# Kernel tuning notes

Measured on AMD Instinct MI355X. Metric: run time of the kernel, lower is better.

## Reference

```python
import jax, jax.numpy as jnp
import numpy as np

B, T_SRC, T_TGT, C_IN, C_OUT = 8, 4096, 2048, 1024, 1024
LN_EPS = 1e-5


def _prefix_mask(lens, T):
    return (jnp.arange(T)[None, :] < lens[:, None]).astype(jnp.int32)


def setup_inputs() -> dict:
    key = jax.random.key(0)
    ks = jax.random.split(key, 6)
    src = jax.random.normal(ks[0], (B, T_SRC, C_IN), dtype=jnp.float32)
    tgt = jax.random.normal(ks[1], (B, T_TGT, C_IN), dtype=jnp.float32)
    # ragged prefix lengths; first row full so src_sizes.max() == T_SRC (static result width)
    src_lens = jax.random.randint(ks[2], (B,), T_SRC // 2, T_SRC + 1).at[0].set(T_SRC)
    tgt_lens = jax.random.randint(ks[3], (B,), T_TGT // 2, T_TGT + 1).at[0].set(T_TGT)
    src_mask = _prefix_mask(src_lens, T_SRC)
    tgt_mask = _prefix_mask(tgt_lens, T_TGT)
    conv_w = jax.random.normal(ks[4], (C_OUT, C_IN), dtype=jnp.float32) * 0.02
    conv_b = jax.random.normal(ks[5], (C_OUT,), dtype=jnp.float32) * 0.02
    ln_g = jnp.ones((C_OUT,), dtype=jnp.float32)
    ln_b = jnp.zeros((C_OUT,), dtype=jnp.float32)
    return {"src": src, "src_mask": src_mask, "tgt": tgt, "tgt_mask": tgt_mask,
            "conv_w": conv_w, "conv_b": conv_b, "ln_g": ln_g, "ln_b": ln_b}


def reference(src, src_mask, tgt, tgt_mask, conv_w, conv_b, ln_g, ln_b):
    # kernel-size-1 Conv1d == per-token linear: [B,T_tgt,C_in] @ W^T + b
    y = jnp.einsum("btc,oc->bto", tgt, conv_w) + conv_b  # [B, T_tgt, C_out]

    src_sizes = src_mask.sum(-1).astype(jnp.int32)  # [B]
    tgt_sizes = tgt_mask.sum(-1).astype(jnp.int32)  # [B]

    # Batched nearest-neighbor ragged resize: out pos j maps to floor(j*tgt/src)
    j = jnp.arange(src.shape[1], dtype=jnp.int32)  # [T_src]
    safe_src = jnp.maximum(src_sizes, 1)[:, None]
    idx = (j[None, :] * tgt_sizes[:, None]) // safe_src  # [B, T_src]
    idx = jnp.clip(idx, 0, jnp.maximum(tgt_sizes, 1)[:, None] - 1)
    gathered = jnp.take_along_axis(y, idx[:, :, None], axis=1)  # [B, T_src, C_out]
    valid = (j[None, :] < src_sizes[:, None])[:, :, None]
    upsampled = jnp.where(valid, gathered, 0.0)

    # LayerNorm over channel dim (applied to all positions, incl. zero padding, as in torch)
    mu = upsampled.mean(-1, keepdims=True)
    var = jnp.mean(jnp.square(upsampled - mu), axis=-1, keepdims=True)
    out = (upsampled - mu) * jax.lax.rsqrt(var + LN_EPS) * ln_g + ln_b
    return (out, src_mask)
```

## Files before the change

kernel.cpp:

```cpp
#include <hip/hip_runtime.h>

#define NB   8
#define TSRC 4096
#define TTGT 2048
#define CH   1024
#define BK   64

typedef __attribute__((ext_vector_type(4))) float  f32x4;
typedef __attribute__((ext_vector_type(8))) __bf16 bf16x8;
typedef __attribute__((ext_vector_type(4))) __bf16 bf16x4;

__device__ __forceinline__ void async16(const void* g, void* l) {
  __builtin_amdgcn_global_load_lds((const __attribute__((address_space(1))) void*)g,
                                   (__attribute__((address_space(3))) void*)l, 16, 0, 0);
}

__global__ __launch_bounds__(256) void prep_kernel(const float* __restrict__ W,
                                                   const int* __restrict__ src_mask,
                                                   const int* __restrict__ tgt_mask,
                                                   __bf16* __restrict__ Wbf,
                                                   int* __restrict__ sizes,
                                                   float* __restrict__ mask_out) {
  const int bx = blockIdx.x;
  const int t  = threadIdx.x;
  if (bx < CH) {
    const float4 v = ((const float4*)(W + (size_t)bx * CH))[t];
    bf16x4 u = {(__bf16)v.x, (__bf16)v.y, (__bf16)v.z, (__bf16)v.w};
    *(bf16x4*)(Wbf + (size_t)bx * CH + t * 4) = u;
  } else if (bx < CH + 16) {
    const int id = bx - CH;
    const int b  = id & 7;
    const int* m = (id < 8) ? (src_mask + (size_t)b * TSRC) : (tgt_mask + (size_t)b * TTGT);
    const int T  = (id < 8) ? TSRC : TTGT;
    int s = 0;
    for (int i = t; i < T; i += 256) s += m[i];
#pragma unroll
    for (int off = 32; off > 0; off >>= 1) s += __shfl_down(s, off);
    __shared__ int red[4];
    if ((t & 63) == 0) red[t >> 6] = s;
    __syncthreads();
    if (t == 0) sizes[id] = red[0] + red[1] + red[2] + red[3];
  } else {
    const int i = (bx - (CH + 16)) * 256 + t;
    mask_out[i] = (float)src_mask[i];
  }
}

__global__ __launch_bounds__(256) void gemm_kernel(const float* __restrict__ A32,
                                                   const __bf16* __restrict__ Bw,
                                                   const float* __restrict__ bias,
                                                   const int* __restrict__ sizes,
                                                   __bf16* __restrict__ y) {
  const int bid = blockIdx.x;
  const int Mt  = bid & 127;
  const int Nt  = bid >> 7;
  const int n0 = Nt * 128;
  const int m0 = Mt * 128;
  const int b  = m0 >> 11;
  const int t0 = m0 & (TTGT - 1);
  if (t0 >= sizes[8 + b]) return;

  __shared__ __bf16 As[128 * BK];
  __shared__ __bf16 Bs[128 * BK];

  const int tid  = threadIdx.x;
  const int lane = tid & 63;
  const int wave = tid >> 6;
  const int wm   = (wave >> 1) * 64;
  const int wn   = (wave & 1) * 64;
  const int lr   = lane & 15;
  const int quad = lane >> 4;

  const int srow = tid >> 3;
  const int scol = (tid & 7) * 8;
  const float*  gA = A32 + (size_t)(m0 + srow) * CH + scol;
  const __bf16* gB = Bw  + (size_t)(n0 + srow) * CH + scol;
  __bf16* lA = As + tid * 8;
  __bf16* lB = Bs + tid * 8;

  f32x4 acc[4][4];
  const f32x4 z = {0.f, 0.f, 0.f, 0.f};
#pragma unroll
  for (int i = 0; i < 4; ++i)
#pragma unroll
    for (int j = 0; j < 4; ++j) acc[i][j] = z;

  float4 a0[4], a1[4];

#pragma unroll
  for (int q = 0; q < 4; ++q) {
    const float* p = gA + (size_t)q * 32 * CH;
    a0[q] = *(const float4*)p;
    a1[q] = *(const float4*)(p + 4);
  }
#pragma unroll
  for (int q = 0; q < 4; ++q) {
    bf16x8 u = {(__bf16)a0[q].x, (__bf16)a0[q].y, (__bf16)a0[q].z, (__bf16)a0[q].w,
                (__bf16)a1[q].x, (__bf16)a1[q].y, (__bf16)a1[q].z, (__bf16)a1[q].w};
    *(bf16x8*)(lA + q * 2048) = u;
  }
#pragma unroll
  for (int q = 0; q < 4; ++q) async16(gB + (size_t)q * 32 * CH, lB + q * 2048);
  __syncthreads();

  for (int kt = 0; kt < CH / BK; ++kt) {
    const int nkb  = (kt + 1) * BK;
    const bool more = (nkb < CH);
    if (more) {
#pragma unroll
      for (int q = 0; q < 4; ++q) {
        const float* p = gA + (size_t)q * 32 * CH + nkb;
        a0[q] = *(const float4*)p;
        a1[q] = *(const float4*)(p + 4);
      }
    }
#pragma unroll
    for (int ko = 0; ko < 2; ++ko) {
      bf16x8 af[4], bf[4];
#pragma unroll
      for (int i = 0; i < 4; ++i)
        af[i] = *(const bf16x8*)(As + (wm + i * 16 + lr) * BK + ko * 32 + quad * 8);
#pragma unroll
      for (int j = 0; j < 4; ++j)
        bf[j] = *(const bf16x8*)(Bs + (wn + j * 16 + lr) * BK + ko * 32 + quad * 8);
#pragma unroll
      for (int i = 0; i < 4; ++i)
#pragma unroll
        for (int j = 0; j < 4; ++j)
          acc[i][j] = __builtin_amdgcn_mfma_f32_16x16x32_bf16(af[i], bf[j], acc[i][j], 0, 0, 0);
    }
    __syncthreads();
    if (more) {
#pragma unroll
      for (int q = 0; q < 4; ++q) {
        bf16x8 u = {(__bf16)a0[q].x, (__bf16)a0[q].y, (__bf16)a0[q].z, (__bf16)a0[q].w,
                    (__bf16)a1[q].x, (__bf16)a1[q].y, (__bf16)a1[q].z, (__bf16)a1[q].w};
        *(bf16x8*)(lA + q * 2048) = u;
      }
#pragma unroll
      for (int q = 0; q < 4; ++q) async16(gB + (size_t)q * 32 * CH + nkb, lB + q * 2048);
    }
    __syncthreads();
  }

#pragma unroll
  for (int i = 0; i < 4; ++i) {
    const int mrow = m0 + wm + i * 16 + quad * 4;
#pragma unroll
    for (int j = 0; j < 4; ++j) {
      const int ncol = n0 + wn + j * 16 + lr;
      const float bv = bias[ncol];
      __bf16* yp = y + (size_t)mrow * CH + ncol;
#pragma unroll
      for (int r = 0; r < 4; ++r) yp[(size_t)r * CH] = (__bf16)(acc[i][j][r] + bv);
    }
  }
}

__global__ __launch_bounds__(256) void ln_kernel(const __bf16* __restrict__ y,
                                                 const int* __restrict__ sizes,
                                                 const float* __restrict__ g,
                                                 const float* __restrict__ be,
                                                 float* __restrict__ out) {
  const int wid = (blockIdx.x * 256 + threadIdx.x) >> 6;
  const int l   = threadIdx.x & 63;
#pragma unroll
  for (int rr = 0; rr < 4; ++rr) {
    const int row = wid + rr * 8192;
    const int b   = row >> 12;
    const int j   = row & (TSRC - 1);
    const int ss  = sizes[b];
    const int tg  = sizes[8 + b];
    float v[16];
    if (j < ss) {
      const int den = (ss > 0) ? ss : 1;
      int ii = (int)(((long long)j * (long long)tg) / den);
      const int hi = ((tg > 1) ? tg : 1) - 1;
      ii = (ii > hi) ? hi : ((ii < 0) ? 0 : ii);
      const __bf16* yr = y + ((size_t)b * TTGT + ii) * CH;
      const bf16x8 u0 = *(const bf16x8*)(yr + l * 8);
      const bf16x8 u1 = *(const bf16x8*)(yr + 512 + l * 8);
#pragma unroll
      for (int k = 0; k < 8; ++k) { v[k] = (float)u0[k]; v[8 + k] = (float)u1[k]; }
    } else {
#pragma unroll
      for (int k = 0; k < 16; ++k) v[k] = 0.f;
    }
    float s = 0.f, q = 0.f;
#pragma unroll
    for (int k = 0; k < 16; ++k) { s += v[k]; q += v[k] * v[k]; }
#pragma unroll
    for (int off = 32; off > 0; off >>= 1) {
      s += __shfl_xor(s, off);
      q += __shfl_xor(q, off);
    }
    const float mu = s * (1.0f / CH);
    float var = q * (1.0f / CH) - mu * mu;
    var = fmaxf(var, 0.0f);
    const float rs = rsqrtf(var + 1e-5f);
    float* orow = out + (size_t)row * CH;
#pragma unroll
    for (int h = 0; h < 2; ++h) {
      const int base = h * 512 + l * 8;
      const float4 g0 = *(const float4*)(g + base);
      const float4 g1 = *(const float4*)(g + base + 4);
      const float4 b0 = *(const float4*)(be + base);
      const float4 b1 = *(const float4*)(be + base + 4);
      float4 o0, o1;
      o0.x = (v[h * 8 + 0] - mu) * rs * g0.x + b0.x;
      o0.y = (v[h * 8 + 1] - mu) * rs * g0.y + b0.y;
      o0.z = (v[h * 8 + 2] - mu) * rs * g0.z + b0.z;
      o0.w = (v[h * 8 + 3] - mu) * rs * g0.w + b0.w;
      o1.x = (v[h * 8 + 4] - mu) * rs * g1.x + b1.x;
      o1.y = (v[h * 8 + 5] - mu) * rs * g1.y + b1.y;
      o1.z = (v[h * 8 + 6] - mu) * rs * g1.z + b1.z;
      o1.w = (v[h * 8 + 7] - mu) * rs * g1.w + b1.w;
      *(float4*)(orow + base)     = o0;
      *(float4*)(orow + base + 4) = o1;
    }
  }
}

__global__ __launch_bounds__(256) void fallback_kernel(const float* __restrict__ tgt,
                                                       const int* __restrict__ src_mask,
                                                       const int* __restrict__ tgt_mask,
                                                       const float* __restrict__ W,
                                                       const float* __restrict__ bias,
                                                       const float* __restrict__ g,
                                                       const float* __restrict__ be,
                                                       float* __restrict__ out,
                                                       float* __restrict__ mask_out) {
  const int bx = blockIdx.x;
  const int b  = bx >> 12;
  const int j  = bx & (TSRC - 1);
  const int t  = threadIdx.x;
  int s1 = 0, s2 = 0;
  for (int i = t; i < TSRC; i += 256) s1 += src_mask[(size_t)b * TSRC + i];
  for (int i = t; i < TTGT; i += 256) s2 += tgt_mask[(size_t)b * TTGT + i];
#pragma unroll
  for (int off = 32; off > 0; off >>= 1) { s1 += __shfl_down(s1, off); s2 += __shfl_down(s2, off); }
  __shared__ int ired[8];
  if ((t & 63) == 0) { ired[t >> 6] = s1; ired[4 + (t >> 6)] = s2; }
  __syncthreads();
  const int ss = ired[0] + ired[1] + ired[2] + ired[3];
  const int tg = ired[4] + ired[5] + ired[6] + ired[7];
  const bool valid = j < ss;
  int ii = 0;
  if (valid) {
    const int den = (ss > 0) ? ss : 1;
    ii = (int)(((long long)j * (long long)tg) / den);
    const int hi = ((tg > 1) ? tg : 1) - 1;
    if (ii > hi) ii = hi;
    if (ii < 0) ii = 0;
  }
  __shared__ float trow[CH];
  const float* tr = tgt + ((size_t)b * TTGT + ii) * CH;
  for (int i = t; i < CH; i += 256) trow[i] = valid ? tr[i] : 0.0f;
  __syncthreads();
  float4 v = make_float4(0.f, 0.f, 0.f, 0.f);
  if (valid) {
    float a0 = 0.f, a1 = 0.f, a2 = 0.f, a3 = 0.f;
    const float* w0 = W + (size_t)(4 * t + 0) * CH;
    const float* w1 = W + (size_t)(4 * t + 1) * CH;
    const float* w2 = W + (size_t)(4 * t + 2) * CH;
    const float* w3 = W + (size_t)(4 * t + 3) * CH;
    for (int k = 0; k < CH; ++k) {
      const float x = trow[k];
      a0 += x * w0[k]; a1 += x * w1[k]; a2 += x * w2[k]; a3 += x * w3[k];
    }
    v.x = a0 + bias[4 * t + 0];
    v.y = a1 + bias[4 * t + 1];
    v.z = a2 + bias[4 * t + 2];
    v.w = a3 + bias[4 * t + 3];
  }
  float s  = v.x + v.y + v.z + v.w;
  float sq = v.x * v.x + v.y * v.y + v.z * v.z + v.w * v.w;
#pragma unroll
  for (int off = 32; off > 0; off >>= 1) {
    s  += __shfl_down(s, off);
    sq += __shfl_down(sq, off);
  }
  __shared__ float red[8];
  __shared__ float stats[2];
  if ((t & 63) == 0) { red[t >> 6] = s; red[4 + (t >> 6)] = sq; }
  __syncthreads();
  if (t == 0) {
    const float S  = red[0] + red[1] + red[2] + red[3];
    const float Q  = red[4] + red[5] + red[6] + red[7];
    const float mu = S * (1.0f / CH);
    float var = Q * (1.0f / CH) - mu * mu;
    var = fmaxf(var, 0.0f);
    stats[0] = mu;
    stats[1] = rsqrtf(var + 1e-5f);
  }
  __syncthreads();
  const float mu = stats[0], rs = stats[1];
  const float4 gg = ((const float4*)g)[t];
  const float4 bb = ((const float4*)be)[t];
  float4 o;
  o.x = (v.x - mu) * rs * gg.x + bb.x;
  o.y = (v.y - mu) * rs * gg.y + bb.y;
  o.z = (v.z - mu) * rs * gg.z + bb.z;
  o.w = (v.w - mu) * rs * gg.w + bb.w;
  ((float4*)(out + ((size_t)b * TSRC + j) * CH))[t] = o;
  if (t == 0) mask_out[bx] = (float)src_mask[bx];
}

extern "C" void kernel_launch(void* const* d_in, const int* in_sizes, int n_in,
                              void* d_out, int out_size, void* d_ws, size_t ws_size,
                              hipStream_t stream) {
  (void)in_sizes; (void)n_in; (void)out_size;
  const int*   src_mask = (const int*)d_in[1];
  const float* tgt      = (const float*)d_in[2];
  const int*   tgt_mask = (const int*)d_in[3];
  const float* conv_w   = (const float*)d_in[4];
  const float* conv_b   = (const float*)d_in[5];
  const float* ln_g     = (const float*)d_in[6];
  const float* ln_b     = (const float*)d_in[7];

  float* out      = (float*)d_out;
  float* mask_out = out + (size_t)NB * TSRC * CH;

  const size_t M       = (size_t)NB * TTGT;
  const size_t off_wbf = 256;
  const size_t off_y   = off_wbf + (size_t)CH * CH * 2;
  const size_t need    = off_y + M * CH * 2;

  if (ws_size >= need) {
    int*    sizes = (int*)d_ws;
    __bf16* Wbf   = (__bf16*)((char*)d_ws + off_wbf);
    __bf16* y     = (__bf16*)((char*)d_ws + off_y);
    prep_kernel<<<CH + 16 + 128, 256, 0, stream>>>(conv_w, src_mask, tgt_mask,
                                                   Wbf, sizes, mask_out);
    gemm_kernel<<<1024, 256, 0, stream>>>(tgt, Wbf, conv_b, sizes, y);
    ln_kernel<<<2048, 256, 0, stream>>>(y, sizes, ln_g, ln_b, out);
  } else {
    fallback_kernel<<<NB * TSRC, 256, 0, stream>>>(tgt, src_mask, tgt_mask, conv_w, conv_b,
                                                   ln_g, ln_b, out, mask_out);
  }
}
```

Before: 330.3 us.

## Load fp32 A tile directly to LDS asynchronously and convert at fragment read

The A operand (fp32 activations) was previously loaded into registers, converted to bf16 and stored to LDS with software prefetch of the next tile. It is now copied as fp32 straight into LDS with global_load_lds, and the conversion to bf16 happens when each wave reads its MFMA fragments. The register-prefetch pipeline is removed, so each K step now issues its loads and waits on a barrier before computing, with no overlap. LDS use for A doubles and the conversion is repeated by both waves that share each A row block.

Measured after the change: 358.4 us. 1.08x slower.

```diff
diff --git a/kernel.cpp b/kernel.cpp
--- a/kernel.cpp
+++ b/kernel.cpp
@@ -60,7 +60,7 @@
   const int t0 = m0 & (TTGT - 1);
   if (t0 >= sizes[8 + b]) return;
 
-  __shared__ __bf16 As[128 * BK];
+  __shared__ float  As[128 * BK];
   __shared__ __bf16 Bs[128 * BK];
 
   const int tid  = threadIdx.x;
@@ -71,11 +71,13 @@
   const int lr   = lane & 15;
   const int quad = lane >> 4;
 
-  const int srow = tid >> 3;
-  const int scol = (tid & 7) * 8;
-  const float*  gA = A32 + (size_t)(m0 + srow) * CH + scol;
-  const __bf16* gB = Bw  + (size_t)(n0 + srow) * CH + scol;
-  __bf16* lA = As + tid * 8;
+  const int arow = tid >> 4;
+  const int acol = (tid & 15) * 4;
+  const float* gA = A32 + (size_t)(m0 + arow) * CH + acol;
+  float* lA = As + tid * 4;
+  const int brow = tid >> 3;
+  const int bcol = (tid & 7) * 8;
+  const __bf16* gB = Bw + (size_t)(n0 + brow) * CH + bcol;
   __bf16* lB = Bs + tid * 8;
 
   f32x4 acc[4][4];
@@ -85,41 +87,27 @@
 #pragma unroll
     for (int j = 0; j < 4; ++j) acc[i][j] = z;
 
-  float4 a0[4], a1[4];
-
-#pragma unroll
-  for (int q = 0; q < 4; ++q) {
-    const float* p = gA + (size_t)q * 32 * CH;
-    a0[q] = *(const float4*)p;
-    a1[q] = *(const float4*)(p + 4);
-  }
-#pragma unroll
-  for (int q = 0; q < 4; ++q) {
-    bf16x8 u = {(__bf16)a0[q].x, (__bf16)a0[q].y, (__bf16)a0[q].z, (__bf16)a0[q].w,
-                (__bf16)a1[q].x, (__bf16)a1[q].y, (__bf16)a1[q].z, (__bf16)a1[q].w};
-    *(bf16x8*)(lA + q * 2048) = u;
-  }
-#pragma unroll
-  for (int q = 0; q < 4; ++q) async16(gB + (size_t)q * 32 * CH, lB + q * 2048);
-  __syncthreads();
-
-  for (int kt = 0; kt < CH / BK; ++kt) {
-    const int nkb  = (kt + 1) * BK;
-    const bool more = (nkb < CH);
-    if (more) {
-#pragma unroll
-      for (int q = 0; q < 4; ++q) {
-        const float* p = gA + (size_t)q * 32 * CH + nkb;
-        a0[q] = *(const float4*)p;
-        a1[q] = *(const float4*)(p + 4);
-      }
-    }
+  for (int kb = 0; kb < CH; kb += BK) {
+#pragma unroll
+    for (int q = 0; q < 8; ++q)
+      async16(gA + (size_t)q * 16 * CH + kb, lA + q * 1024);
+#pragma unroll
+    for (int q = 0; q < 4; ++q)
+      async16(gB + (size_t)q * 32 * CH + kb, lB + q * 2048);
+    __syncthreads();
 #pragma unroll
     for (int ko = 0; ko < 2; ++ko) {
       bf16x8 af[4], bf[4];
 #pragma unroll
-      for (int i = 0; i < 4; ++i)
-        af[i] = *(const bf16x8*)(As + (wm + i * 16 + lr) * BK + ko * 32 + quad * 8);
+      for (int i = 0; i < 4; ++i) {
+        const float* ap = As + (wm + i * 16 + lr) * BK + ko * 32 + quad * 8;
+        const f32x4 v0 = *(const f32x4*)ap;
+        const f32x4 v1 = *(const f32x4*)(ap + 4);
+        bf16x8 a;
+#pragma unroll
+        for (int k = 0; k < 4; ++k) { a[k] = (__bf16)v0[k]; a[4 + k] = (__bf16)v1[k]; }
+        af[i] = a;
+      }
 #pragma unroll
       for (int j = 0; j < 4; ++j)
         bf[j] = *(const bf16x8*)(Bs + (wn + j * 16 + lr) * BK + ko * 32 + quad * 8);
@@ -128,17 +116,6 @@
 #pragma unroll
         for (int j = 0; j < 4; ++j)
           acc[i][j] = __builtin_amdgcn_mfma_f32_16x16x32_bf16(af[i], bf[j], acc[i][j], 0, 0, 0);
-    }
-    __syncthreads();
-    if (more) {
-#pragma unroll
-      for (int q = 0; q < 4; ++q) {
-        bf16x8 u = {(__bf16)a0[q].x, (__bf16)a0[q].y, (__bf16)a0[q].z, (__bf16)a0[q].w,
-                    (__bf16)a1[q].x, (__bf16)a1[q].y, (__bf16)a1[q].z, (__bf16)a1[q].w};
-        *(bf16x8*)(lA + q * 2048) = u;
-      }
-#pragma unroll
-      for (int q = 0; q < 4; ++q) async16(gB + (size_t)q * 32 * CH + nkb, lB + q * 2048);
     }
     __syncthreads();
   }
```
